# Kernel optimization log

Hardware: AMD Instinct MI355X
Metric: run time of the kernel (lower is better)

## Reference

```python
import jax, jax.numpy as jnp
import numpy as np

DN = ('NCH', 'OIH', 'NCH')

def conv1d(x, w, b, pad):
    y = jax.lax.conv_general_dilated(x, w, (1,), [(pad, pad)], dimension_numbers=DN)
    return y if b is None else y + b[None, :, None]

def bn_eval(x, g, b, m, v, eps):
    s = g * jax.lax.rsqrt(v + eps)
    return x * s[None, :, None] + (b - m * s)[None, :, None]

def swish(x):
    return x * jax.nn.sigmoid(x)

def setup_inputs() -> dict:
    key = jax.random.key(0)
    ks = jax.random.split(key, 8)
    B, T, P = 16, 8192, 32
    inp = {
        'x': jax.random.normal(ks[0], (B, 1, T), jnp.float32),
        'conv_w': jax.random.normal(ks[1], (512, 1, 9), jnp.float32) * 0.1,
        'bn_g': jnp.ones((512,), jnp.float32),
        'bn_b': jnp.zeros((512,), jnp.float32),
        'bn_m': jnp.zeros((512,), jnp.float32),
        'bn_v': jnp.ones((512,), jnp.float32),
        'p1_w': jax.random.normal(ks[2], (P, 2, 31), jnp.float32) * 0.1,
        'p1_b': jnp.zeros((P,), jnp.float32),
        'pbn1_g': jnp.ones((P,), jnp.float32),
        'pbn1_b': jnp.zeros((P,), jnp.float32),
        'pbn1_m': jnp.zeros((P,), jnp.float32),
        'pbn1_v': jnp.ones((P,), jnp.float32),
        'p2_w': jax.random.normal(ks[3], (P, P, 15), jnp.float32) * 0.05,
        'p2_b': jnp.zeros((P,), jnp.float32),
        'pbn2_g': jnp.ones((P,), jnp.float32),
        'pbn2_b': jnp.zeros((P,), jnp.float32),
        'pbn2_m': jnp.zeros((P,), jnp.float32),
        'pbn2_v': jnp.ones((P,), jnp.float32),
        'p3_w': jax.random.normal(ks[4], (2, P, 15), jnp.float32) * 0.001,  # source scales last conv weight by 0.01
        'p3_b': jnp.full((2,), -np.log(2.0), jnp.float32),                 # source sets bias to -log(2)
        'norm_mean': jnp.ones((1,), jnp.float32),                           # eval-mode renorm buffer
    }
    return inp

def reference(x, conv_w, bn_g, bn_b, bn_m, bn_v,
              p1_w, p1_b, pbn1_g, pbn1_b, pbn1_m, pbn1_v,
              p2_w, p2_b, pbn2_g, pbn2_b, pbn2_m, pbn2_v,
              p3_w, p3_b, norm_mean):
    B, _, T = x.shape
    # main conv -> BN(eps=1e-3) -> GLU(dim=1); dropout is identity in eval
    h = conv1d(x, conv_w, None, 9 // 2)                 # [B, 512, T]
    h = bn_eval(h, bn_g, bn_b, bn_m, bn_v, 1e-3)
    a, g = jnp.split(h, 2, axis=1)
    features = a * jax.nn.sigmoid(g)                    # [B, 256, T]
    # predictor on cat([x, x*x])
    j = conv1d(jnp.concatenate([x, x * x], axis=1), p1_w, p1_b, 15)
    j = swish(bn_eval(j, pbn1_g, pbn1_b, pbn1_m, pbn1_v, 1e-5))
    j = conv1d(j, p2_w, p2_b, 7)
    j = swish(bn_eval(j, pbn2_g, pbn2_b, pbn2_m, pbn2_v, 1e-5))
    j = conv1d(j, p3_w, p3_b, 7)                        # [B, 2, T]
    weights = jax.nn.sigmoid(j[:, 0, :])                # [B, T]
    moves = jax.nn.sigmoid(j[:, 1, :])
    bmoves = moves
    moves = moves * norm_mean[0]                        # eval: renorm = norm_mean buffer
    # CIF-style dynamic pooling (row_pool), vectorized over batch
    feats = jnp.transpose(features, (0, 2, 1))          # [B, T, C]
    fw = feats * weights[..., None]
    poses = jnp.cumsum(jax.lax.stop_gradient(moves), axis=1)  # moves.detach() in source
    floors = jnp.floor(poses)
    w1 = 1.0 - (poses - floors)
    w2 = poses - floors
    fl = floors.astype(jnp.int32)
    ce = fl + 1
    Lmax = T + 2  # static bound: poses <= T so ceil index <= T+1
    C = fw.shape[2]
    def pool(fw_i, fl_i, ce_i, w1_i, w2_i):
        out = jnp.zeros((Lmax, C), fw_i.dtype)
        out = out.at[fl_i].add(w1_i[:, None] * fw_i)
        out = out.at[ce_i].add(w2_i[:, None] * fw_i)
        return out
    x_evs = jax.vmap(pool)(fw, fl, ce, w1, w2)          # [B, Lmax, C]
    lens = fl[:, -1] + 2                                 # int(ceils[-1]) + 1
    x_evs = jnp.transpose(x_evs, (0, 2, 1))             # [B, C, Lmax]
    pad = 3 - (Lmax % 3)
    x_evs = jnp.pad(x_evs, ((0, 0), (0, 0), (0, pad)))
    return x_evs, lens, bmoves, weights
```

## Files before the change

kernel.cpp:

```cpp
#include <hip/hip_runtime.h>
#include <math.h>

static constexpr int TT = 8192;
static constexpr int LFULL = 8196;
static constexpr int BSTRIDE = LFULL + 2;

static constexpr size_t XE_OFF   = 0;
static constexpr size_t LENS_OFF = (size_t)16*256*LFULL;
static constexpr size_t BM_OFF   = LENS_OFF + 16;
static constexpr size_t WT_OFF   = BM_OFF + (size_t)16*TT;

static constexpr size_t U_OFF     = 0;
static constexpr size_t V_OFF     = U_OFF + (size_t)16*32*TT;
static constexpr size_t MOVES_OFF = V_OFF + (size_t)16*32*TT;
static constexpr size_t C1_OFF    = MOVES_OFF + (size_t)16*TT;
static constexpr size_t C2_OFF    = C1_OFF + (size_t)16*TT;
static constexpr size_t BND_OFF   = U_OFF;

__device__ __forceinline__ float sig_(float z) { return 1.0f / (1.0f + __expf(-z)); }

typedef float f4v __attribute__((ext_vector_type(4)));
typedef float f2v __attribute__((ext_vector_type(2)));
__device__ __forceinline__ void nt_store4(float* p, float a, float b, float c, float d) {
    f4v v = {a, b, c, d};
    __builtin_nontemporal_store(v, (f4v*)p);
}

static constexpr int UPS = 572;
static constexpr int VS  = 276;

__global__ __launch_bounds__(512, 2) void k_convall(
    const float* __restrict__ x,
    const float* __restrict__ p1w, const float* __restrict__ p1b,
    const float* __restrict__ g1, const float* __restrict__ b1,
    const float* __restrict__ m1, const float* __restrict__ v1,
    const float* __restrict__ p2w, const float* __restrict__ p2b,
    const float* __restrict__ g2, const float* __restrict__ b2,
    const float* __restrict__ m2, const float* __restrict__ v2,
    const float* __restrict__ p3w, const float* __restrict__ p3b,
    const float* __restrict__ nm,
    float* __restrict__ outw, float* __restrict__ outbm, float* __restrict__ moves)
{
    __shared__ __align__(16) float xin[320];
    __shared__ __align__(16) float w1t[2 * 992];
    __shared__ __align__(16) float uld[16 * UPS + 4];
    __shared__ __align__(16) float w2t[16 * 1024];
    __shared__ __align__(16) float wsh[960];
    const int tid = threadIdx.x;
    const int b = blockIdx.y;
    const int t0 = blockIdx.x * 256;

    if (tid < 320) {
        int id = t0 - 29 + tid;
        xin[tid] = (id >= 0 && id < TT) ? x[b * TT + id] : 0.f;
    }
#pragma unroll
    for (int it = 0; it < 4; ++it) {
        int idx = it * 512 + tid;
        if (idx < 1984) {
            int c = idx / 62; int r = idx - c * 62; int ci = r / 31; int k = r - ci * 31;
            w1t[ci * 992 + c * 31 + k] = p1w[idx];
        }
    }
#pragma unroll
    for (int it = 0; it < 32; ++it) {
        int idx = it * 512 + tid;
        int p = idx >> 10; int r = idx & 1023; int oc = r >> 5; int m = r & 31;
        int k = m >> 1, par = m & 1;
        float val = (k < 15) ? p2w[oc * 480 + (2 * p + par) * 15 + k] : 0.f;
        int phys = (p << 10) + (oc << 5) + ((((m >> 2) ^ (oc & 7)) << 2) | (m & 3));
        w2t[phys] = val;
    }
    { if (tid < 960 - 512) wsh[512 + tid] = p3w[512 + tid]; if (tid < 512) wsh[tid] = p3w[tid]; }
    __syncthreads();

    {
        const int cB = tid & 31, pg = tid >> 5;
        const float s1v = g1[cB] * rsqrtf(v1[cB] + 1e-5f);
        const float sh1 = b1[cB] - m1[cB] * s1v;
        const float bias1 = p1b[cB];
        const int base = pg * 20;
        const float* wA = &w1t[cB * 31];
        const float* wB = &w1t[992 + cB * 31];
        float* urow = &uld[(cB >> 1) * UPS + (cB & 1)];
#pragma unroll
        for (int h = 0; h < 3; ++h) {
            const int off = h * 8;
            const int len = (h < 2) ? 8 : 4;
            const int nld = (h < 2) ? 10 : 9;
            const int ul0 = base + off;
            if (ul0 < 284) {
                float win[40], wsq[40];
                const float4* xp = (const float4*)(&xin[ul0]);
#pragma unroll
                for (int r = 0; r < 10; ++r) {
                    if (r < nld) {
                        float4 q = xp[r];
                        win[4*r] = q.x; win[4*r+1] = q.y; win[4*r+2] = q.z; win[4*r+3] = q.w;
                    }
                }
#pragma unroll
                for (int i = 0; i < 40; ++i) { if (i < 4 * nld) wsq[i] = win[i] * win[i]; }
                float acc[8];
#pragma unroll
                for (int i = 0; i < 8; ++i) acc[i] = bias1;
#pragma unroll
                for (int k = 0; k < 31; ++k) {
                    const float a = wA[k], bw = wB[k];
#pragma unroll
                    for (int i = 0; i < 8; ++i) {
                        if (i < len) {
                            acc[i] = fmaf(a, win[i + k], acc[i]);
                            acc[i] = fmaf(bw, wsq[i + k], acc[i]);
                        }
                    }
                }
#pragma unroll
                for (int i = 0; i < 8; ++i) {
                    if (i < len && ul0 + i < 284) {
                        const float z = fmaf(acc[i], s1v, sh1);
                        urow[(ul0 + i) * 2] = z * sig_(z);
                    }
                }
            }
        }
    }
    __syncthreads();

    const int cl = tid & 31;
    const int tg = tid >> 5;

    float o[16];
    {
        f2v accP[16];
#pragma unroll
        for (int i = 0; i < 16; ++i) accP[i] = f2v{0.f, 0.f};
        for (int p = 0; p < 16; ++p) {
            f2v win2[32];
            const float4* wp = (const float4*)(&uld[p * UPS + tg * 32]);
#pragma unroll
            for (int r = 0; r < 16; ++r) {
                float4 q = wp[r];
                win2[2*r]   = f2v{q.x, q.y};
                win2[2*r+1] = f2v{q.z, q.w};
            }
            f2v w2f[16];
            const float* wrow = &w2t[(p << 10) + (cl << 5)];
#pragma unroll
            for (int r = 0; r < 8; ++r) {
                float4 q = *(const float4*)(&wrow[((r ^ (cl & 7)) << 2)]);
                w2f[2*r]   = f2v{q.x, q.y};
                w2f[2*r+1] = f2v{q.z, q.w};
            }
#pragma unroll
            for (int k = 0; k < 15; ++k)
#pragma unroll
                for (int i = 0; i < 16; ++i)
                    accP[i] = __builtin_elementwise_fma(win2[i + k], w2f[k], accP[i]);
        }
        const float bias2 = p2b[cl];
        const float s = g2[cl] * rsqrtf(v2[cl] + 1e-5f);
        const float sh = b2[cl] - m2[cl] * s;
        const int tvb = t0 - 7 + tg * 16;
#pragma unroll
        for (int i = 0; i < 16; ++i) {
            const float a2 = accP[i].x + accP[i].y + bias2;
            const float z = fmaf(a2, s, sh);
            const float vvv = z * sig_(z);
            const int tv = tvb + i;
            o[i] = (tv >= 0 && tv < TT) ? vvv : 0.f;
        }
    }

    const int lane = tid & 63, wv = tid >> 6;
    const int ocT = ((wv & 1) << 4) + (lane & 15);
    const int sub = lane >> 4;
    const int vl0 = 256 + ((wv >> 1) << 2);
    float vt[4];
    {
        f2v accT[4];
#pragma unroll
        for (int i = 0; i < 4; ++i) accT[i] = f2v{0.f, 0.f};
#pragma unroll
        for (int j = 0; j < 4; ++j) {
            const int p = sub + 4 * j;
            f2v win2[20];
            const float4* wp = (const float4*)(&uld[p * UPS + vl0 * 2]);
#pragma unroll
            for (int r = 0; r < 10; ++r) {
                float4 q = wp[r];
                win2[2*r]   = f2v{q.x, q.y};
                win2[2*r+1] = f2v{q.z, q.w};
            }
            f2v w2f[16];
            const float* wrow = &w2t[(p << 10) + (ocT << 5)];
#pragma unroll
            for (int r = 0; r < 8; ++r) {
                float4 q = *(const float4*)(&wrow[((r ^ (ocT & 7)) << 2)]);
                w2f[2*r]   = f2v{q.x, q.y};
                w2f[2*r+1] = f2v{q.z, q.w};
            }
#pragma unroll
            for (int k = 0; k < 15; ++k)
#pragma unroll
                for (int i = 0; i < 4; ++i)
                    accT[i] = __builtin_elementwise_fma(win2[i + k], w2f[k], accT[i]);
        }
        float acc4[4];
#pragma unroll
        for (int i = 0; i < 4; ++i) acc4[i] = accT[i].x + accT[i].y;
#pragma unroll
        for (int i = 0; i < 4; ++i) {
            acc4[i] += __shfl_xor(acc4[i], 16, 64);
            acc4[i] += __shfl_xor(acc4[i], 32, 64);
        }
        const float sT = g2[ocT] * rsqrtf(v2[ocT] + 1e-5f);
        const float shT = b2[ocT] - m2[ocT] * sT;
        const float bT = p2b[ocT];
#pragma unroll
        for (int i = 0; i < 4; ++i) {
            const float z = fmaf(acc4[i] + bT, sT, shT);
            const float vvv = z * sig_(z);
            const int tv = t0 - 7 + vl0 + i;
            vt[i] = (tv >= 0 && tv < TT) ? vvv : 0.f;
        }
    }
    __syncthreads();

    {
        float* vbuf = uld;
#pragma unroll
        for (int r = 0; r < 4; ++r) {
            f4v a = {o[4*r], o[4*r+1], o[4*r+2], o[4*r+3]};
            *(f4v*)&vbuf[cl * VS + tg * 16 + 4 * r] = a;
        }
        if (sub == 0) {
            f4v a = {vt[0], vt[1], vt[2], vt[3]};
            *(f4v*)&vbuf[ocT * VS + vl0] = a;
        }
    }
    __syncthreads();

    {
        const float* vbuf = uld;
        const int g = tid >> 3;
        const int q3 = tid & 7;
        float acc[8];
#pragma unroll
        for (int i = 0; i < 8; ++i) acc[i] = 0.f;
#pragma unroll
        for (int i = 0; i < 4; ++i) {
            const int ci = q3 + 8 * i;
            float win[20];
            const float4* wp = (const float4*)(&vbuf[ci * VS + g * 4]);
#pragma unroll
            for (int r = 0; r < 5; ++r) {
                float4 v4 = wp[r];
                win[4*r] = v4.x; win[4*r+1] = v4.y; win[4*r+2] = v4.z; win[4*r+3] = v4.w;
            }
            const float* w0 = &wsh[ci * 15];
            const float* w1p = &wsh[480 + ci * 15];
#pragma unroll
            for (int k = 0; k < 15; ++k) {
                const float a = w0[k], gw = w1p[k];
#pragma unroll
                for (int t4 = 0; t4 < 4; ++t4) {
                    acc[t4]     = fmaf(a,  win[k + t4], acc[t4]);
                    acc[4 + t4] = fmaf(gw, win[k + t4], acc[4 + t4]);
                }
            }
        }
#pragma unroll
        for (int i = 0; i < 8; ++i) {
            acc[i] += __shfl_xor(acc[i], 1, 64);
            acc[i] += __shfl_xor(acc[i], 2, 64);
            acc[i] += __shfl_xor(acc[i], 4, 64);
        }
        if (q3 == 0) {
            const float nmv = nm[0];
            const float b0 = p3b[0], b1v = p3b[1];
            const int t = t0 + g * 4;
            float4 wvv = make_float4(sig_(acc[0]+b0), sig_(acc[1]+b0), sig_(acc[2]+b0), sig_(acc[3]+b0));
            float4 bm = make_float4(sig_(acc[4]+b1v), sig_(acc[5]+b1v), sig_(acc[6]+b1v), sig_(acc[7]+b1v));
            float4 mv = make_float4(bm.x*nmv, bm.y*nmv, bm.z*nmv, bm.w*nmv);
            *(float4*)&outw[b * TT + t]  = wvv;
            *(float4*)&outbm[b * TT + t] = bm;
            *(float4*)&moves[b * TT + t] = mv;
        }
    }
}

__global__ __launch_bounds__(1024) void k_scan(
    const float* __restrict__ moves, const float* __restrict__ wts,
    float* __restrict__ coef1, float* __restrict__ coef2,
    int* __restrict__ bnd, float* __restrict__ lens)
{
    __shared__ float wsum[16];
    const int tid = threadIdx.x;
    const int b = blockIdx.x;
    const int lane = tid & 63, wv = tid >> 6;
    float carry = 0.f;

    int* bb = &bnd[b * BSTRIDE];
    for (int i = tid; i < BSTRIDE; i += 1024) bb[i] = TT;
    if (tid == 0) { bb[0] = 0; bb[1] = 0; }
    __syncthreads();

    const float4* mv4 = (const float4*)&moves[b * TT];
    const float4* wt4 = (const float4*)&wts[b * TT];
    float4* c14 = (float4*)&coef1[b * TT];
    float4* c24 = (float4*)&coef2[b * TT];

    for (int chunk = 0; chunk < 2; ++chunk) {
        const int idx = chunk * 1024 + tid;
        float4 m = mv4[idx];
        const float s = m.x + m.y + m.z + m.w;
        float v = s;
#pragma unroll
        for (int off = 1; off < 64; off <<= 1) {
            float n = __shfl_up(v, off, 64);
            if (lane >= off) v += n;
        }
        if (lane == 63) wsum[wv] = v;
        __syncthreads();
        float pre = carry;
        for (int w = 0; w < wv; ++w) pre += wsum[w];
        float tot = 0.f;
#pragma unroll
        for (int w = 0; w < 16; ++w) tot += wsum[w];
        const float base = pre + (v - s);
        const float p0 = base + m.x;
        const float p1 = p0 + m.y;
        const float p2 = p1 + m.z;
        const float p3 = p2 + m.w;
        const float4 w4 = wt4[idx];
        const float fr0 = p0 - floorf(p0), fr1 = p1 - floorf(p1);
        const float fr2 = p2 - floorf(p2), fr3 = p3 - floorf(p3);
        c14[idx] = make_float4((1.f - fr0) * w4.x, (1.f - fr1) * w4.y,
                               (1.f - fr2) * w4.z, (1.f - fr3) * w4.w);
        c24[idx] = make_float4(fr0 * w4.x, fr1 * w4.y, fr2 * w4.z, fr3 * w4.w);
        {
            int lf = (int)floorf(base) + 1;
            const int lfe = (int)floorf(p3);
            const int tbase = idx << 2;
            for (; lf <= lfe; ++lf) {
                const float lff = (float)lf;
                int t = tbase;
                if (p0 >= lff) { }
                else if (p1 >= lff) t += 1;
                else if (p2 >= lff) t += 2;
                else t += 3;
                if (lf + 1 < BSTRIDE) bb[lf + 1] = t;
            }
        }
        if (chunk == 1 && tid == 1023) lens[b] = floorf(p3) + 2.0f;
        carry += tot;
        __syncthreads();
    }
}

static constexpr int LTILE = 32;
static constexpr int CHK = 256;
static constexpr int NPOOLX = (LFULL + LTILE - 1) / LTILE;

__global__ __launch_bounds__(256) void k_pool(
    const float* __restrict__ x,
    const float* __restrict__ cw,
    const float* __restrict__ bng, const float* __restrict__ bnb,
    const float* __restrict__ bnm, const float* __restrict__ bnv,
    const float* __restrict__ coef1, const float* __restrict__ coef2,
    const int* __restrict__ bnd, const float* __restrict__ lens,
    float* __restrict__ xevs)
{
    __shared__ float out_lds[256 * 33];
    __shared__ float4 xl4[68];
    __shared__ float4 c1l4[CHK / 4], c2l4[CHK / 4];
    __shared__ int lbs[LTILE + 2];
    float* xl = (float*)xl4;
    float* c1l = (float*)c1l4;
    float* c2l = (float*)c2l4;

    const int tid = threadIdx.x;
    const int b = blockIdx.y;

    if (blockIdx.x >= NPOOLX) {
        const int zx = blockIdx.x - NPOOLX;
        const int zs = (((int)lens[b]) + 15) & ~15;
        if (zs >= LFULL) return;
        const int n4 = (LFULL - zs) >> 2;
        for (int r = 0; r < 4; ++r) {
            float* row = &xevs[((size_t)(b * 256 + zx * 4 + r)) * LFULL + zs];
            for (int i = tid; i < n4; i += 256) nt_store4(row + 4 * i, 0.f, 0.f, 0.f, 0.f);
        }
        return;
    }

    const int l0 = blockIdx.x * LTILE;
    const int LTa = min(LTILE, LFULL - l0);

    if (tid < LTa + 2) lbs[tid] = bnd[b * BSTRIDE + l0 + tid];
    __syncthreads();

    const int t_lo = lbs[0];
    const int t_hi = lbs[LTa + 1];
    if (t_lo >= t_hi) return;

    const size_t rowbase = (size_t)b * 256 * LFULL + l0;

#pragma unroll
    for (int li = 0; li < 33; ++li) out_lds[tid * 33 + li] = 0.f;

    const int c = tid;
    float wa[9], wg[9];
#pragma unroll
    for (int k = 0; k < 9; ++k) { wa[k] = cw[c * 9 + k]; wg[k] = cw[(c + 256) * 9 + k]; }
    const float sa = bng[c] * rsqrtf(bnv[c] + 1e-3f);
    const float sha = bnb[c] - bnm[c] * sa;
    const float sg = bng[c + 256] * rsqrtf(bnv[c + 256] + 1e-3f);
    const float shg = bnb[c + 256] - bnm[c + 256] * sg;

    const float* xg = &x[b * TT];
    const float* c1g = &coef1[b * TT];
    const float* c2g = &coef2[b * TT];

    float accA = 0.f, accB = 0.f;
    int j = 0;
    int nb = lbs[1];

    for (int cs = t_lo; cs < t_hi; cs += CHK) {
        const int ce = min(cs + CHK, t_hi);
        const int len = ce - cs;
        __syncthreads();
        for (int idx = tid; idx < len + 12; idx += 256) {
            int id = cs - 4 + idx;
            xl[idx] = (id >= 0 && id < TT) ? xg[id] : 0.f;
        }
        if (tid < len) { c1l[tid] = c1g[cs + tid]; c2l[tid] = c2g[cs + tid]; }
        __syncthreads();

        const int len4 = len >> 2;
        for (int g = 0; g < len4; ++g) {
            float4 A = xl4[g], Bq = xl4[g + 1], Cq = xl4[g + 2];
            float w[12] = {A.x, A.y, A.z, A.w, Bq.x, Bq.y, Bq.z, Bq.w, Cq.x, Cq.y, Cq.z, Cq.w};
            float f[4];
#pragma unroll
            for (int i = 0; i < 4; ++i) {
                float s0 = 0.f, s1 = 0.f;
#pragma unroll
                for (int k = 0; k < 9; ++k) { s0 = fmaf(wa[k], w[i + k], s0); s1 = fmaf(wg[k], w[i + k], s1); }
                const float av = fmaf(s0, sa, sha);
                const float gv = fmaf(s1, sg, shg);
                f[i] = av * sig_(gv);
            }
            float4 c1v = c1l4[g], c2v = c2l4[g];
            const float c1a[4] = {c1v.x, c1v.y, c1v.z, c1v.w};
            const float c2a[4] = {c2v.x, c2v.y, c2v.z, c2v.w};
            const int tb = cs + (g << 2);
#pragma unroll
            for (int i = 0; i < 4; ++i) {
                const int t = tb + i;
                while (t >= nb) {
                    int li = j - 1;
                    if (li >= 0 && li < LTa) out_lds[c * 33 + li] = accA;
                    accA = accB; accB = 0.f;
                    ++j;
                    nb = lbs[j + 1];
                }
                accA = fmaf(c1a[i], f[i], accA);
                accB = fmaf(c2a[i], f[i], accB);
            }
        }
        for (int t = cs + (len4 << 2); t < ce; ++t) {
            const int il = t - cs;
            float s0 = 0.f, s1 = 0.f;
#pragma unroll
            for (int k = 0; k < 9; ++k) { float xv = xl[il + k]; s0 = fmaf(wa[k], xv, s0); s1 = fmaf(wg[k], xv, s1); }
            const float av = fmaf(s0, sa, sha);
            const float gv = fmaf(s1, sg, shg);
            const float f0 = av * sig_(gv);
            while (t >= nb) {
                int li = j - 1;
                if (li >= 0 && li < LTa) out_lds[c * 33 + li] = accA;
                accA = accB; accB = 0.f;
                ++j;
                nb = lbs[j + 1];
            }
            accA = fmaf(c1l[il], f0, accA);
            accB = fmaf(c2l[il], f0, accB);
        }
    }
    {
        int li = j - 1;
        if (li >= 0 && li < LTa) out_lds[c * 33 + li] = accA;
    }
    __syncthreads();

#pragma unroll
    for (int it = 0; it < 8; ++it) {
        int idx4 = it * 256 + tid;
        int cc = idx4 >> 3, q = (idx4 & 7) << 2;
        if (q < LTa) {
            nt_store4(&xevs[rowbase + (size_t)cc * LFULL + q],
                      out_lds[cc * 33 + q + 0], out_lds[cc * 33 + q + 1],
                      out_lds[cc * 33 + q + 2], out_lds[cc * 33 + q + 3]);
        }
    }
}

extern "C" void kernel_launch(void* const* d_in, const int* in_sizes, int n_in,
                              void* d_out, int out_size, void* d_ws, size_t ws_size,
                              hipStream_t stream) {
    (void)in_sizes; (void)n_in; (void)out_size; (void)ws_size;
    const float* x      = (const float*)d_in[0];
    const float* conv_w = (const float*)d_in[1];
    const float* bn_g   = (const float*)d_in[2];
    const float* bn_b   = (const float*)d_in[3];
    const float* bn_m   = (const float*)d_in[4];
    const float* bn_v   = (const float*)d_in[5];
    const float* p1_w   = (const float*)d_in[6];
    const float* p1_b   = (const float*)d_in[7];
    const float* pbn1_g = (const float*)d_in[8];
    const float* pbn1_b = (const float*)d_in[9];
    const float* pbn1_m = (const float*)d_in[10];
    const float* pbn1_v = (const float*)d_in[11];
    const float* p2_w   = (const float*)d_in[12];
    const float* p2_b   = (const float*)d_in[13];
    const float* pbn2_g = (const float*)d_in[14];
    const float* pbn2_b = (const float*)d_in[15];
    const float* pbn2_m = (const float*)d_in[16];
    const float* pbn2_v = (const float*)d_in[17];
    const float* p3_w   = (const float*)d_in[18];
    const float* p3_b   = (const float*)d_in[19];
    const float* nm     = (const float*)d_in[20];

    float* out = (float*)d_out;
    float* ws  = (float*)d_ws;
    float* moves = ws + MOVES_OFF;
    float* coef1 = ws + C1_OFF;
    float* coef2 = ws + C2_OFF;
    int*   bnd   = (int*)(ws + BND_OFF);
    float* xevs  = out + XE_OFF;
    float* lens  = out + LENS_OFF;
    float* bmv   = out + BM_OFF;
    float* wts   = out + WT_OFF;

    k_convall<<<dim3(32, 16), 512, 0, stream>>>(
        x, p1_w, p1_b, pbn1_g, pbn1_b, pbn1_m, pbn1_v,
        p2_w, p2_b, pbn2_g, pbn2_b, pbn2_m, pbn2_v,
        p3_w, p3_b, nm, wts, bmv, moves);
    k_scan<<<16, 1024, 0, stream>>>(moves, wts, coef1, coef2, bnd, lens);
    k_pool<<<dim3(NPOOLX + 64, 16), 256, 0, stream>>>(
        x, conv_w, bn_g, bn_b, bn_m, bn_v, coef1, coef2, bnd, lens, xevs);
}
```

Measured before the change: 312.0 us.

## Precompute conv2 weight layout in global memory and drop LDS weight staging

A small prep kernel rearranges the p2 conv weights once into a global buffer in the padded, parity-interleaved order. The fused conv kernel then reads its weights straight from global/L1 instead of staging a 64KB swizzled copy in LDS every block. This frees LDS so the launch bound can rise from 2 to 4 blocks per CU. The u-activation LDS layout is also changed to 16-element chunks with padding, and the thread-to-(channel, time) mapping is swapped so each thread reads two adjacent chunks. In exchange there is one extra kernel launch and per-thread weight loads from global memory instead of LDS.

```diff
diff --git a/kernel.cpp b/kernel.cpp
--- a/kernel.cpp
+++ b/kernel.cpp
@@ -16,6 +16,7 @@
 static constexpr size_t C1_OFF    = MOVES_OFF + (size_t)16*TT;
 static constexpr size_t C2_OFF    = C1_OFF + (size_t)16*TT;
 static constexpr size_t BND_OFF   = U_OFF;
+static constexpr size_t W2G_OFF   = V_OFF;
 
 __device__ __forceinline__ float sig_(float z) { return 1.0f / (1.0f + __expf(-z)); }
 
@@ -26,15 +27,28 @@
     __builtin_nontemporal_store(v, (f4v*)p);
 }
 
-static constexpr int UPS = 572;
-static constexpr int VS  = 276;
-
-__global__ __launch_bounds__(512, 2) void k_convall(
+__global__ __launch_bounds__(512) void k_prep(const float* __restrict__ p2w,
+                                              float* __restrict__ w2g)
+{
+    const int idx = blockIdx.x * 512 + threadIdx.x;
+    const int par = idx & 1;
+    const int k   = (idx >> 1) & 15;
+    const int oc  = (idx >> 5) & 31;
+    const int p   = idx >> 10;
+    w2g[idx] = (k < 15) ? p2w[oc * 480 + (2 * p + par) * 15 + k] : 0.f;
+}
+
+static constexpr int UROW = 648;
+static constexpr int VS   = 276;
+
+__device__ __forceinline__ int cidx_(int ul) { return (ul >> 4) * 36 + ((ul & 15) << 1); }
+
+__global__ __launch_bounds__(512, 4) void k_convall(
     const float* __restrict__ x,
     const float* __restrict__ p1w, const float* __restrict__ p1b,
     const float* __restrict__ g1, const float* __restrict__ b1,
     const float* __restrict__ m1, const float* __restrict__ v1,
-    const float* __restrict__ p2w, const float* __restrict__ p2b,
+    const float* __restrict__ w2g, const float* __restrict__ p2b,
     const float* __restrict__ g2, const float* __restrict__ b2,
     const float* __restrict__ m2, const float* __restrict__ v2,
     const float* __restrict__ p3w, const float* __restrict__ p3b,
@@ -43,8 +57,7 @@
 {
     __shared__ __align__(16) float xin[320];
     __shared__ __align__(16) float w1t[2 * 992];
-    __shared__ __align__(16) float uld[16 * UPS + 4];
-    __shared__ __align__(16) float w2t[16 * 1024];
+    __shared__ __align__(16) float uld[16 * UROW + 8];
     __shared__ __align__(16) float wsh[960];
     const int tid = threadIdx.x;
     const int b = blockIdx.y;
@@ -61,15 +74,6 @@
             int c = idx / 62; int r = idx - c * 62; int ci = r / 31; int k = r - ci * 31;
             w1t[ci * 992 + c * 31 + k] = p1w[idx];
         }
-    }
-#pragma unroll
-    for (int it = 0; it < 32; ++it) {
-        int idx = it * 512 + tid;
-        int p = idx >> 10; int r = idx & 1023; int oc = r >> 5; int m = r & 31;
-        int k = m >> 1, par = m & 1;
-        float val = (k < 15) ? p2w[oc * 480 + (2 * p + par) * 15 + k] : 0.f;
-        int phys = (p << 10) + (oc << 5) + ((((m >> 2) ^ (oc & 7)) << 2) | (m & 3));
-        w2t[phys] = val;
     }
     { if (tid < 960 - 512) wsh[512 + tid] = p3w[512 + tid]; if (tid < 512) wsh[tid] = p3w[tid]; }
     __syncthreads();
@@ -82,7 +86,7 @@
         const int base = pg * 20;
         const float* wA = &w1t[cB * 31];
         const float* wB = &w1t[992 + cB * 31];
-        float* urow = &uld[(cB >> 1) * UPS + (cB & 1)];
+        float* urow = &uld[(cB >> 1) * UROW + (cB & 1)];
 #pragma unroll
         for (int h = 0; h < 3; ++h) {
             const int off = h * 8;
@@ -119,7 +123,7 @@
                 for (int i = 0; i < 8; ++i) {
                     if (i < len && ul0 + i < 284) {
                         const float z = fmaf(acc[i], s1v, sh1);
-                        urow[(ul0 + i) * 2] = z * sig_(z);
+                        urow[cidx_(ul0 + i)] = z * sig_(z);
                     }
                 }
             }
@@ -127,8 +131,8 @@
     }
     __syncthreads();
 
-    const int cl = tid & 31;
-    const int tg = tid >> 5;
+    const int cl = tid >> 4;
+    const int tg = tid & 15;
 
     float o[16];
     {
@@ -137,26 +141,36 @@
         for (int i = 0; i < 16; ++i) accP[i] = f2v{0.f, 0.f};
         for (int p = 0; p < 16; ++p) {
             f2v win2[32];
-            const float4* wp = (const float4*)(&uld[p * UPS + tg * 32]);
-#pragma unroll
-            for (int r = 0; r < 16; ++r) {
-                float4 q = wp[r];
+            const float4* cp0 = (const float4*)(&uld[p * UROW + tg * 36]);
+            const float4* cp1 = (const float4*)(&uld[p * UROW + (tg + 1) * 36]);
+#pragma unroll
+            for (int r = 0; r < 8; ++r) {
+                float4 q = cp0[r];
                 win2[2*r]   = f2v{q.x, q.y};
                 win2[2*r+1] = f2v{q.z, q.w};
             }
-            f2v w2f[16];
-            const float* wrow = &w2t[(p << 10) + (cl << 5)];
 #pragma unroll
             for (int r = 0; r < 8; ++r) {
-                float4 q = *(const float4*)(&wrow[((r ^ (cl & 7)) << 2)]);
-                w2f[2*r]   = f2v{q.x, q.y};
-                w2f[2*r+1] = f2v{q.z, q.w};
-            }
-#pragma unroll
-            for (int k = 0; k < 15; ++k)
+                float4 q = cp1[r];
+                win2[16+2*r]   = f2v{q.x, q.y};
+                win2[16+2*r+1] = f2v{q.z, q.w};
+            }
+            const float4* wrow = (const float4*)(w2g + (((p << 5) + cl) << 5));
+#pragma unroll
+            for (int r8 = 0; r8 < 8; ++r8) {
+                float4 wq = wrow[r8];
+                const int k0 = 2 * r8;
+                const f2v wv0 = {wq.x, wq.y};
 #pragma unroll
                 for (int i = 0; i < 16; ++i)
-                    accP[i] = __builtin_elementwise_fma(win2[i + k], w2f[k], accP[i]);
+                    accP[i] = __builtin_elementwise_fma(win2[i + k0], wv0, accP[i]);
+                if (r8 < 7) {
+                    const f2v wv1 = {wq.z, wq.w};
+#pragma unroll
+                    for (int i = 0; i < 16; ++i)
+                        accP[i] = __builtin_elementwise_fma(win2[i + k0 + 1], wv1, accP[i]);
+                }
+            }
         }
         const float bias2 = p2b[cl];
         const float s = g2[cl] * rsqrtf(v2[cl] + 1e-5f);
@@ -185,26 +199,26 @@
         for (int j = 0; j < 4; ++j) {
             const int p = sub + 4 * j;
             f2v win2[20];
-            const float4* wp = (const float4*)(&uld[p * UPS + vl0 * 2]);
-#pragma unroll
-            for (int r = 0; r < 10; ++r) {
-                float4 q = wp[r];
-                win2[2*r]   = f2v{q.x, q.y};
-                win2[2*r+1] = f2v{q.z, q.w};
-            }
-            f2v w2f[16];
-            const float* wrow = &w2t[(p << 10) + (ocT << 5)];
-#pragma unroll
-            for (int r = 0; r < 8; ++r) {
-                float4 q = *(const float4*)(&wrow[((r ^ (ocT & 7)) << 2)]);
-                w2f[2*r]   = f2v{q.x, q.y};
-                w2f[2*r+1] = f2v{q.z, q.w};
-            }
-#pragma unroll
-            for (int k = 0; k < 15; ++k)
+            const float* prow = &uld[p * UROW];
+#pragma unroll
+            for (int jj = 0; jj < 20; ++jj)
+                win2[jj] = *(const f2v*)&prow[cidx_(vl0 + jj)];
+            const float4* wrow = (const float4*)(w2g + (((p << 5) + ocT) << 5));
+#pragma unroll
+            for (int r8 = 0; r8 < 8; ++r8) {
+                float4 wq = wrow[r8];
+                const int k0 = 2 * r8;
+                const f2v wv0 = {wq.x, wq.y};
 #pragma unroll
                 for (int i = 0; i < 4; ++i)
-                    accT[i] = __builtin_elementwise_fma(win2[i + k], w2f[k], accT[i]);
+                    accT[i] = __builtin_elementwise_fma(win2[i + k0], wv0, accT[i]);
+                if (r8 < 7) {
+                    const f2v wv1 = {wq.z, wq.w};
+#pragma unroll
+                    for (int i = 0; i < 4; ++i)
+                        accT[i] = __builtin_elementwise_fma(win2[i + k0 + 1], wv1, accT[i]);
+                }
+            }
         }
         float acc4[4];
 #pragma unroll
@@ -539,14 +553,16 @@
     float* coef1 = ws + C1_OFF;
     float* coef2 = ws + C2_OFF;
     int*   bnd   = (int*)(ws + BND_OFF);
+    float* w2g   = ws + W2G_OFF;
     float* xevs  = out + XE_OFF;
     float* lens  = out + LENS_OFF;
     float* bmv   = out + BM_OFF;
     float* wts   = out + WT_OFF;
 
+    k_prep<<<dim3(32), 512, 0, stream>>>(p2_w, w2g);
     k_convall<<<dim3(32, 16), 512, 0, stream>>>(
         x, p1_w, p1_b, pbn1_g, pbn1_b, pbn1_m, pbn1_v,
-        p2_w, p2_b, pbn2_g, pbn2_b, pbn2_m, pbn2_v,
+        w2g, p2_b, pbn2_g, pbn2_b, pbn2_m, pbn2_v,
         p3_w, p3_b, nm, wts, bmv, moves);
     k_scan<<<16, 1024, 0, stream>>>(moves, wts, coef1, coef2, bnd, lens);
     k_pool<<<dim3(NPOOLX + 64, 16), 256, 0, stream>>>(
```

Result: slower. 318.4 us (+2.1%).
